# Performance work log

Hardware: AMD Instinct MI355X
Metric: run time of the kernel (lower is better)

## Reference

```python
import jax, jax.numpy as jnp
import numpy as np

# Clause structure: 4 unary clauses and 4 binary (joined-space) clauses,
# each with 3 literals; first literal negated ('n' prefix).
U_IDX = np.array([[0, 1, 2], [3, 4, 5], [6, 7, 8], [9, 10, 11]], dtype=np.int32)
U_SIGNS = np.array([[-1.0, 1.0, 1.0]] * 4, dtype=np.float32)
# Joined matrix columns: [u[i1] (0..15), u[i2] (16..31), binary (32..35)]
B_IDX = np.array([[0, 16, 32], [1, 17, 33], [2, 18, 34], [3, 19, 35]], dtype=np.int32)
B_SIGNS = np.array([[-1.0, 1.0, 1.0]] * 4, dtype=np.float32)

N_NODES, N_UNARY = 50000, 16
N_EDGES, N_BINARY = 1600000, 4
INIT_W = 0.5


def setup_inputs() -> dict:
    key = jax.random.key(0)
    k1, k2, k3, k4 = jax.random.split(key, 4)
    unary = jax.random.normal(k1, (N_NODES, N_UNARY), dtype=jnp.float32)
    binary = jax.random.normal(k2, (N_EDGES, N_BINARY), dtype=jnp.float32)
    edge_index = jax.random.randint(k3, (2, N_EDGES), 0, N_NODES, dtype=jnp.int32)
    wu = jnp.full((4,), INIT_W, dtype=jnp.float32)  # learnable unary clause weights
    wb = jnp.full((4,), INIT_W, dtype=jnp.float32)  # learnable binary clause weights
    return {"unary": unary, "binary": binary, "wu": wu, "wb": wb, "edge_index": edge_index}


def _knowledge_enhancer(x, idx, signs, w):
    """x: [R, P]; idx/signs: [C, L]; w: [C]. Returns summed deltas [R, P]."""
    lit = x[:, idx] * signs                                    # [R, C, L] signed literals
    d = (w[:, None] * jax.nn.softmax(lit, axis=-1)) * signs    # [R, C, L] signed deltas
    return jnp.zeros_like(x).at[:, idx].add(d)                 # scatter-sum over clauses


def reference(unary, binary, wu, wb, edge_index):
    i1, i2 = edge_index[0], edge_index[1]
    P = unary.shape[1]
    # Unary knowledge enhancement
    u = unary + _knowledge_enhancer(unary, U_IDX, U_SIGNS, wu)
    # Join: per-edge [u[i1] | u[i2] | binary]
    joined = jnp.concatenate([u[i1], u[i2], binary], axis=1)   # [E, 2P+B]
    d = _knowledge_enhancer(joined, B_IDX, B_SIGNS, wb)        # [E, 2P+B]
    # GroupBy: scatter node blocks back, keep binary block
    n = unary.shape[0]
    delta_up = (jax.ops.segment_sum(d[:, :P], i1, num_segments=n)
                + jax.ops.segment_sum(d[:, P:2 * P], i2, num_segments=n))
    delta_bp = d[:, 2 * P:]
    # activation = identity (default)
    return u + delta_up, binary + delta_bp
```

## Files before the change

kernel.cpp:

```cpp
#include <hip/hip_runtime.h>
#include <hip/hip_bf16.h>

#define N_NODES 50000
#define N_UNARY 16
#define N_EDGES 1600000
#define N_BINARY 4

typedef float vfloat4 __attribute__((ext_vector_type(4)));

#define FP_SCALE 127.0f
#define FP_INV   (1.0f / 127.0f)

#define BUCKET_SHIFT 11
#define BUCKET_NODES 2048
#define N_BUCKETS 25
#define N_GROUPS 50
#define SEG_CAP 73728
#define N_CHUNKS 10

#define SCAT_BLOCK 1024
#define SCAT_RECS (2 * SCAT_BLOCK)

#define SEG_BYTES  ((size_t)N_GROUPS * SEG_CAP * 8)
#define PART_BYTES ((size_t)N_GROUPS * N_CHUNKS * BUCKET_NODES * 8)
#define WS_NEEDED  (SEG_BYTES + 256 + PART_BYTES)

__device__ inline void enhance_u4(const float x[6], float wu0, float wu1,
                                  float u[4]) {
    float l0 = -x[0], l1 = x[1], l2 = x[2];
    float m  = fmaxf(l0, fmaxf(l1, l2));
    float e0 = __expf(l0 - m), e1 = __expf(l1 - m), e2 = __expf(l2 - m);
    float inv = 1.0f / (e0 + e1 + e2);
    u[0] = x[0] - wu0 * e0 * inv;
    u[1] = x[1] + wu0 * e1 * inv;
    u[2] = x[2] + wu0 * e2 * inv;
    float l3 = -x[3], l4 = x[4], l5 = x[5];
    float m2 = fmaxf(l3, fmaxf(l4, l5));
    float f0 = __expf(l3 - m2), f1 = __expf(l4 - m2), f2 = __expf(l5 - m2);
    float inv2 = 1.0f / (f0 + f1 + f2);
    u[3] = x[3] - wu1 * f0 * inv2;
}

__device__ inline void edge_math(const float* unary, const float* binary,
                                 float wu0, float wu1, const float wc[4],
                                 int i1, int i2, int e,
                                 float s0[4], float s1[4],
                                 float* out_b) {
    const float4* u1p = (const float4*)(unary + (size_t)i1 * N_UNARY);
    const float4* u2p = (const float4*)(unary + (size_t)i2 * N_UNARY);
    float4 x1a = u1p[0], x1b = u1p[1];
    float4 x2a = u2p[0], x2b = u2p[1];
    float xa[6] = {x1a.x, x1a.y, x1a.z, x1a.w, x1b.x, x1b.y};
    float xb[6] = {x2a.x, x2a.y, x2a.z, x2a.w, x2b.x, x2b.y};
    float a[4], b[4];
    enhance_u4(xa, wu0, wu1, a);
    enhance_u4(xb, wu0, wu1, b);

    vfloat4 bn = __builtin_nontemporal_load((const vfloat4*)binary + e);
    float bb[4] = {bn.x, bn.y, bn.z, bn.w};
    float ob[4];
#pragma unroll
    for (int c = 0; c < 4; ++c) {
        float l0 = -a[c], l1 = b[c], l2 = bb[c];
        float m  = fmaxf(l0, fmaxf(l1, l2));
        float e0 = __expf(l0 - m);
        float e1 = __expf(l1 - m);
        float e2 = __expf(l2 - m);
        float inv = 1.0f / (e0 + e1 + e2);
        s0[c] = e0 * inv;
        s1[c] = e1 * inv;
        ob[c] = bb[c] + wc[c] * e2 * inv;
    }
    vfloat4 obv = {ob[0], ob[1], ob[2], ob[3]};
    __builtin_nontemporal_store(obv, (vfloat4*)out_b + e);
}

__device__ inline unsigned long long make_rec(const float s[4], int local_id) {
    unsigned v0 = __float2uint_rn(s[0] * FP_SCALE);
    unsigned v1 = __float2uint_rn(s[1] * FP_SCALE);
    unsigned v2 = __float2uint_rn(s[2] * FP_SCALE);
    unsigned v3 = __float2uint_rn(s[3] * FP_SCALE);
    unsigned pl = v0 | (v1 << 7) | (v2 << 14) | (v3 << 21);
    return (unsigned long long)pl | ((unsigned long long)(unsigned)local_id << 28);
}

__device__ inline unsigned long long pack4_16(const float s[4]) {
    unsigned long long a = __float2uint_rn(s[0] * FP_SCALE);
    unsigned long long b = __float2uint_rn(s[1] * FP_SCALE);
    unsigned long long c = __float2uint_rn(s[2] * FP_SCALE);
    unsigned long long d = __float2uint_rn(s[3] * FP_SCALE);
    return a | (b << 16) | (c << 32) | (d << 48);
}

__global__ void __launch_bounds__(SCAT_BLOCK)
kenn_edge_scatter_kernel(const float* __restrict__ unary,
                         const float* __restrict__ binary,
                         const float* __restrict__ wu,
                         const float* __restrict__ wb,
                         const int* __restrict__ edge_index,
                         unsigned long long* __restrict__ segs,
                         unsigned* __restrict__ tails,
                         float* __restrict__ out_b) {
    __shared__ unsigned l_cnt[N_GROUPS];
    __shared__ unsigned l_pref[N_GROUPS + 1];
    __shared__ unsigned l_gbase[N_GROUPS];
    __shared__ unsigned long long staged[SCAT_RECS];
    __shared__ unsigned char staged_g[SCAT_RECS];

    int tid = threadIdx.x;
    if (tid < N_GROUPS) l_cnt[tid] = 0;
    __syncthreads();

    int e = blockIdx.x * SCAT_BLOCK + tid;
    bool valid = (e < N_EDGES);

    int g1 = 0, g2 = 0;
    unsigned pos1 = 0, pos2 = 0;
    unsigned long long rec1 = 0, rec2 = 0;

    if (valid) {
        int i1 = __builtin_nontemporal_load(edge_index + e);
        int i2 = __builtin_nontemporal_load(edge_index + N_EDGES + e);
        float wu0 = wu[0], wu1 = wu[1];
        float wc[4] = {wb[0], wb[1], wb[2], wb[3]};
        float s0[4], s1[4];
        edge_math(unary, binary, wu0, wu1, wc, i1, i2, e, s0, s1, out_b);
        rec1 = make_rec(s0, i1 & (BUCKET_NODES - 1));
        rec2 = make_rec(s1, i2 & (BUCKET_NODES - 1));
        g1 = i1 >> BUCKET_SHIFT;
        g2 = N_BUCKETS + (i2 >> BUCKET_SHIFT);
        pos1 = atomicAdd(&l_cnt[g1], 1u);
        pos2 = atomicAdd(&l_cnt[g2], 1u);
    }
    __syncthreads();

    if (tid == 0) {
        unsigned run = 0;
#pragma unroll
        for (int g = 0; g < N_GROUPS; ++g) { l_pref[g] = run; run += l_cnt[g]; }
        l_pref[N_GROUPS] = run;
    } else if (tid >= 64 && tid < 64 + N_GROUPS) {
        int g = tid - 64;
        unsigned c = l_cnt[g];
        l_gbase[g] = c ? atomicAdd(tails + g, c) : 0u;
    }
    __syncthreads();

    if (valid) {
        unsigned s1p = l_pref[g1] + pos1;
        unsigned s2p = l_pref[g2] + pos2;
        staged[s1p] = rec1;  staged_g[s1p] = (unsigned char)g1;
        staged[s2p] = rec2;  staged_g[s2p] = (unsigned char)g2;
    }
    __syncthreads();

    unsigned total = l_pref[N_GROUPS];
    for (unsigned i = tid; i < total; i += SCAT_BLOCK) {
        unsigned g = staged_g[i];
        unsigned long long rec = staged[i];
        unsigned p = l_gbase[g] + (i - l_pref[g]);
        if (p < SEG_CAP)
            __builtin_nontemporal_store(rec, segs + (size_t)g * SEG_CAP + p);
    }
}

__global__ void __launch_bounds__(512)
kenn_reduce_kernel(const unsigned long long* __restrict__ segs,
                   const unsigned* __restrict__ tails,
                   unsigned long long* __restrict__ partials) {
    __shared__ unsigned long long lacc[BUCKET_NODES];
    int chunk = blockIdx.x;
    int g     = blockIdx.y;
    int tid   = threadIdx.x;

    for (int i = tid; i < BUCKET_NODES; i += blockDim.x) lacc[i] = 0ull;
    __syncthreads();

    unsigned cnt = tails[g];
    if (cnt > SEG_CAP) cnt = SEG_CAP;
    unsigned csz   = (cnt + N_CHUNKS - 1) / N_CHUNKS;
    unsigned start = chunk * csz;
    unsigned end   = start + csz;
    if (end > cnt) end = cnt;

    const unsigned long long* seg = segs + (size_t)g * SEG_CAP;
    for (unsigned i = start + tid; i < end; i += blockDim.x) {
        unsigned long long r = seg[i];
        unsigned id = (unsigned)(r >> 28) & (BUCKET_NODES - 1);
        unsigned pl = (unsigned)r & 0x0FFFFFFFu;
        unsigned long long exp =
            (unsigned long long)(pl & 127u) |
            ((unsigned long long)(pl & (127u << 7))  << 9)  |
            ((unsigned long long)(pl & (127u << 14)) << 18) |
            ((unsigned long long)(pl & (127u << 21)) << 27);
        atomicAdd(&lacc[id], exp);
    }
    __syncthreads();

    unsigned long long* dst =
        partials + ((size_t)g * N_CHUNKS + chunk) * BUCKET_NODES;
    for (int i = tid; i < BUCKET_NODES; i += blockDim.x)
        __builtin_nontemporal_store(lacc[i], dst + i);
}

__global__ void kenn_node_final_kernel(const float* __restrict__ unary,
                                       const float* __restrict__ wu,
                                       const float* __restrict__ wb,
                                       const unsigned long long* __restrict__ partials,
                                       const unsigned long long* __restrict__ accN,
                                       const unsigned long long* __restrict__ accP,
                                       int use_partials,
                                       float* __restrict__ out_u) {
    int node = blockIdx.x * blockDim.x + threadIdx.x;
    if (node >= N_NODES) return;

    const float4* up = (const float4*)(unary + (size_t)node * N_UNARY);
    float4 x0 = up[0], x1 = up[1], x2 = up[2], x3 = up[3];
    float x[16] = {x0.x, x0.y, x0.z, x0.w,
                   x1.x, x1.y, x1.z, x1.w,
                   x2.x, x2.y, x2.z, x2.w,
                   x3.x, x3.y, x3.z, x3.w};
    float wuc[4] = {wu[0], wu[1], wu[2], wu[3]};

    float y[16];
#pragma unroll
    for (int i = 0; i < 16; ++i) y[i] = x[i];

#pragma unroll
    for (int c = 0; c < 4; ++c) {
        float l0 = -x[3 * c + 0];
        float l1 =  x[3 * c + 1];
        float l2 =  x[3 * c + 2];
        float m  = fmaxf(l0, fmaxf(l1, l2));
        float e0 = __expf(l0 - m);
        float e1 = __expf(l1 - m);
        float e2 = __expf(l2 - m);
        float inv = 1.0f / (e0 + e1 + e2);
        y[3 * c + 0] -= wuc[c] * e0 * inv;
        y[3 * c + 1] += wuc[c] * e1 * inv;
        y[3 * c + 2] += wuc[c] * e2 * inv;
    }

    unsigned long long pn, pp;
    if (use_partials) {
        int bucket = node >> BUCKET_SHIFT;
        int local  = node & (BUCKET_NODES - 1);
        const unsigned long long* pN =
            partials + ((size_t)bucket * N_CHUNKS) * BUCKET_NODES + local;
        const unsigned long long* pP =
            partials + ((size_t)(N_BUCKETS + bucket) * N_CHUNKS) * BUCKET_NODES + local;
        pn = 0ull; pp = 0ull;
#pragma unroll
        for (int c = 0; c < N_CHUNKS; ++c) {
            pn += pN[(size_t)c * BUCKET_NODES];
            pp += pP[(size_t)c * BUCKET_NODES];
        }
    } else {
        pn = accN[node];
        pp = accP[node];
    }

    float wbc[4] = {wb[0], wb[1], wb[2], wb[3]};
    y[0] += wbc[0] * ((float)(int)((pp      ) & 0xffff) - (float)(int)((pn      ) & 0xffff)) * FP_INV;
    y[1] += wbc[1] * ((float)(int)((pp >> 16) & 0xffff) - (float)(int)((pn >> 16) & 0xffff)) * FP_INV;
    y[2] += wbc[2] * ((float)(int)((pp >> 32) & 0xffff) - (float)(int)((pn >> 32) & 0xffff)) * FP_INV;
    y[3] += wbc[3] * ((float)(int)((pp >> 48) & 0xffff) - (float)(int)((pn >> 48) & 0xffff)) * FP_INV;

    float4* op = (float4*)(out_u + (size_t)node * N_UNARY);
    op[0] = make_float4(y[0],  y[1],  y[2],  y[3]);
    op[1] = make_float4(y[4],  y[5],  y[6],  y[7]);
    op[2] = make_float4(y[8],  y[9],  y[10], y[11]);
    op[3] = make_float4(y[12], y[13], y[14], y[15]);
}

__global__ void kenn_edge_atomic_kernel(const float* __restrict__ unary,
                                        const float* __restrict__ binary,
                                        const float* __restrict__ wu,
                                        const float* __restrict__ wb,
                                        const int* __restrict__ edge_index,
                                        unsigned long long* __restrict__ accN,
                                        unsigned long long* __restrict__ accP,
                                        float* __restrict__ out_b) {
    int e = blockIdx.x * blockDim.x + threadIdx.x;
    if (e >= N_EDGES) return;
    int i1 = __builtin_nontemporal_load(edge_index + e);
    int i2 = __builtin_nontemporal_load(edge_index + N_EDGES + e);
    float wu0 = wu[0], wu1 = wu[1];
    float wc[4] = {wb[0], wb[1], wb[2], wb[3]};
    float s0[4], s1[4];
    edge_math(unary, binary, wu0, wu1, wc, i1, i2, e, s0, s1, out_b);
    atomicAdd(accN + i1, pack4_16(s0));
    atomicAdd(accP + i2, pack4_16(s1));
}

extern "C" void kernel_launch(void* const* d_in, const int* in_sizes, int n_in,
                              void* d_out, int out_size, void* d_ws, size_t ws_size,
                              hipStream_t stream) {
    const float* unary      = (const float*)d_in[0];
    const float* binary     = (const float*)d_in[1];
    const float* wu         = (const float*)d_in[2];
    const float* wb         = (const float*)d_in[3];
    const int*   edge_index = (const int*)d_in[4];

    float* out_u = (float*)d_out;
    float* out_b = (float*)d_out + (size_t)N_NODES * N_UNARY;

    if (ws_size >= WS_NEEDED) {
        unsigned long long* segs = (unsigned long long*)d_ws;
        unsigned* tails = (unsigned*)((char*)d_ws + SEG_BYTES);
        unsigned long long* partials =
            (unsigned long long*)((char*)d_ws + SEG_BYTES + 256);

        (void)hipMemsetAsync(tails, 0, N_GROUPS * sizeof(unsigned), stream);
        {
            dim3 grid((N_EDGES + SCAT_BLOCK - 1) / SCAT_BLOCK);
            kenn_edge_scatter_kernel<<<grid, dim3(SCAT_BLOCK), 0, stream>>>(
                unary, binary, wu, wb, edge_index, segs, tails, out_b);
        }
        {
            dim3 grid(N_CHUNKS, N_GROUPS);
            kenn_reduce_kernel<<<grid, dim3(512), 0, stream>>>(
                segs, tails, partials);
        }
        {
            dim3 block(256);
            dim3 grid((N_NODES + 255) / 256);
            kenn_node_final_kernel<<<grid, block, 0, stream>>>(
                unary, wu, wb, partials, nullptr, nullptr, 1, out_u);
        }
    } else {
        unsigned long long* accN = (unsigned long long*)d_ws;
        unsigned long long* accP = accN + N_NODES;
        (void)hipMemsetAsync(accN, 0,
                             (size_t)N_NODES * 2 * sizeof(unsigned long long),
                             stream);
        {
            dim3 block(256);
            dim3 grid((N_EDGES + 255) / 256);
            kenn_edge_atomic_kernel<<<grid, block, 0, stream>>>(
                unary, binary, wu, wb, edge_index, accN, accP, out_b);
        }
        {
            dim3 block(256);
            dim3 grid((N_NODES + 255) / 256);
            kenn_node_final_kernel<<<grid, block, 0, stream>>>(
                unary, wu, wb, nullptr, accN, accP, 0, out_u);
        }
    }
}
```

Baseline: 150.3 us.

## Precompute enhanced unary node values once and simplify edge scatter kernel

Adds a pre-kernel that computes the four enhanced unary values per node once and stores them as a float4 array. The edge kernel then gathers one 16-byte vector per endpoint instead of redoing the unary softmax for every edge. The same pre-kernel also zeroes the tail counters, which replaces the separate memset. Other changes: the scatter block shrinks to 512 threads, bounds checks are dropped because the edge count divides evenly, the serial prefix sum becomes a wavefront shuffle scan, and the tail counters are padded to separate cache lines. The cost is one extra kernel launch and an extra node-sized buffer in the workspace.

```diff
diff --git a/kernel.cpp b/kernel.cpp
--- a/kernel.cpp
+++ b/kernel.cpp
@@ -18,12 +18,16 @@
 #define SEG_CAP 73728
 #define N_CHUNKS 10
 
-#define SCAT_BLOCK 1024
+#define TAILS_STRIDE 16
+
+#define SCAT_BLOCK 512
 #define SCAT_RECS (2 * SCAT_BLOCK)
 
-#define SEG_BYTES  ((size_t)N_GROUPS * SEG_CAP * 8)
-#define PART_BYTES ((size_t)N_GROUPS * N_CHUNKS * BUCKET_NODES * 8)
-#define WS_NEEDED  (SEG_BYTES + 256 + PART_BYTES)
+#define SEG_BYTES   ((size_t)N_GROUPS * SEG_CAP * 8)
+#define TAILS_BYTES ((size_t)4096)
+#define PART_BYTES  ((size_t)N_GROUPS * N_CHUNKS * BUCKET_NODES * 8)
+#define UE_BYTES    ((size_t)N_NODES * 16)
+#define WS_NEEDED   (SEG_BYTES + TAILS_BYTES + PART_BYTES + UE_BYTES)
 
 __device__ inline void enhance_u4(const float x[6], float wu0, float wu1,
                                   float u[4]) {
@@ -92,17 +96,32 @@
     return a | (b << 16) | (c << 32) | (d << 48);
 }
 
+__global__ void __launch_bounds__(256)
+kenn_pre_kernel(const float* __restrict__ unary,
+                const float* __restrict__ wu,
+                float4* __restrict__ ue,
+                unsigned* __restrict__ tails) {
+    int n = blockIdx.x * blockDim.x + threadIdx.x;
+    if (n < N_GROUPS) tails[n * TAILS_STRIDE] = 0u;
+    if (n >= N_NODES) return;
+    const float4* up = (const float4*)(unary + (size_t)n * N_UNARY);
+    float4 x0 = up[0], x1 = up[1];
+    float x[6] = {x0.x, x0.y, x0.z, x0.w, x1.x, x1.y};
+    float u[4];
+    enhance_u4(x, wu[0], wu[1], u);
+    ue[n] = make_float4(u[0], u[1], u[2], u[3]);
+}
+
 __global__ void __launch_bounds__(SCAT_BLOCK)
-kenn_edge_scatter_kernel(const float* __restrict__ unary,
+kenn_edge_scatter_kernel(const float4* __restrict__ ue,
                          const float* __restrict__ binary,
-                         const float* __restrict__ wu,
                          const float* __restrict__ wb,
                          const int* __restrict__ edge_index,
                          unsigned long long* __restrict__ segs,
                          unsigned* __restrict__ tails,
                          float* __restrict__ out_b) {
     __shared__ unsigned l_cnt[N_GROUPS];
-    __shared__ unsigned l_pref[N_GROUPS + 1];
+    __shared__ unsigned l_pref[N_GROUPS];
     __shared__ unsigned l_gbase[N_GROUPS];
     __shared__ unsigned long long staged[SCAT_RECS];
     __shared__ unsigned char staged_g[SCAT_RECS];
@@ -112,50 +131,66 @@
     __syncthreads();
 
     int e = blockIdx.x * SCAT_BLOCK + tid;
-    bool valid = (e < N_EDGES);
-
-    int g1 = 0, g2 = 0;
-    unsigned pos1 = 0, pos2 = 0;
-    unsigned long long rec1 = 0, rec2 = 0;
-
-    if (valid) {
-        int i1 = __builtin_nontemporal_load(edge_index + e);
-        int i2 = __builtin_nontemporal_load(edge_index + N_EDGES + e);
-        float wu0 = wu[0], wu1 = wu[1];
-        float wc[4] = {wb[0], wb[1], wb[2], wb[3]};
-        float s0[4], s1[4];
-        edge_math(unary, binary, wu0, wu1, wc, i1, i2, e, s0, s1, out_b);
-        rec1 = make_rec(s0, i1 & (BUCKET_NODES - 1));
-        rec2 = make_rec(s1, i2 & (BUCKET_NODES - 1));
-        g1 = i1 >> BUCKET_SHIFT;
-        g2 = N_BUCKETS + (i2 >> BUCKET_SHIFT);
-        pos1 = atomicAdd(&l_cnt[g1], 1u);
-        pos2 = atomicAdd(&l_cnt[g2], 1u);
-    }
-    __syncthreads();
-
-    if (tid == 0) {
-        unsigned run = 0;
-#pragma unroll
-        for (int g = 0; g < N_GROUPS; ++g) { l_pref[g] = run; run += l_cnt[g]; }
-        l_pref[N_GROUPS] = run;
+    int i1 = __builtin_nontemporal_load(edge_index + e);
+    int i2 = __builtin_nontemporal_load(edge_index + N_EDGES + e);
+
+    float4 av = ue[i1];
+    float4 bv = ue[i2];
+    float a[4] = {av.x, av.y, av.z, av.w};
+    float b[4] = {bv.x, bv.y, bv.z, bv.w};
+    vfloat4 bn = __builtin_nontemporal_load((const vfloat4*)binary + e);
+    float bb[4] = {bn.x, bn.y, bn.z, bn.w};
+    float wc[4] = {wb[0], wb[1], wb[2], wb[3]};
+
+    float s0[4], s1[4], ob[4];
+#pragma unroll
+    for (int c = 0; c < 4; ++c) {
+        float l0 = -a[c], l1 = b[c], l2 = bb[c];
+        float m  = fmaxf(l0, fmaxf(l1, l2));
+        float e0 = __expf(l0 - m);
+        float e1 = __expf(l1 - m);
+        float e2 = __expf(l2 - m);
+        float inv = 1.0f / (e0 + e1 + e2);
+        s0[c] = e0 * inv;
+        s1[c] = e1 * inv;
+        ob[c] = bb[c] + wc[c] * e2 * inv;
+    }
+    vfloat4 obv = {ob[0], ob[1], ob[2], ob[3]};
+    __builtin_nontemporal_store(obv, (vfloat4*)out_b + e);
+
+    unsigned long long rec1 = make_rec(s0, i1 & (BUCKET_NODES - 1));
+    unsigned long long rec2 = make_rec(s1, i2 & (BUCKET_NODES - 1));
+    int g1 = i1 >> BUCKET_SHIFT;
+    int g2 = N_BUCKETS + (i2 >> BUCKET_SHIFT);
+    unsigned pos1 = atomicAdd(&l_cnt[g1], 1u);
+    unsigned pos2 = atomicAdd(&l_cnt[g2], 1u);
+    __syncthreads();
+
+    if (tid < 64) {
+        unsigned c = (tid < N_GROUPS) ? l_cnt[tid] : 0u;
+        unsigned s = c;
+#pragma unroll
+        for (int off = 1; off < 64; off <<= 1) {
+            unsigned o = __shfl_up(s, off, 64);
+            if (tid >= off) s += o;
+        }
+        if (tid < N_GROUPS) l_pref[tid] = s - c;
     } else if (tid >= 64 && tid < 64 + N_GROUPS) {
         int g = tid - 64;
         unsigned c = l_cnt[g];
-        l_gbase[g] = c ? atomicAdd(tails + g, c) : 0u;
-    }
-    __syncthreads();
-
-    if (valid) {
-        unsigned s1p = l_pref[g1] + pos1;
-        unsigned s2p = l_pref[g2] + pos2;
-        staged[s1p] = rec1;  staged_g[s1p] = (unsigned char)g1;
-        staged[s2p] = rec2;  staged_g[s2p] = (unsigned char)g2;
-    }
-    __syncthreads();
-
-    unsigned total = l_pref[N_GROUPS];
-    for (unsigned i = tid; i < total; i += SCAT_BLOCK) {
+        l_gbase[g] = c ? atomicAdd(tails + g * TAILS_STRIDE, c) : 0u;
+    }
+    __syncthreads();
+
+    unsigned p1 = l_pref[g1] + pos1;
+    unsigned p2 = l_pref[g2] + pos2;
+    staged[p1] = rec1;  staged_g[p1] = (unsigned char)g1;
+    staged[p2] = rec2;  staged_g[p2] = (unsigned char)g2;
+    __syncthreads();
+
+#pragma unroll
+    for (int k = 0; k < 2; ++k) {
+        unsigned i = (unsigned)tid + k * SCAT_BLOCK;
         unsigned g = staged_g[i];
         unsigned long long rec = staged[i];
         unsigned p = l_gbase[g] + (i - l_pref[g]);
@@ -176,7 +211,7 @@
     for (int i = tid; i < BUCKET_NODES; i += blockDim.x) lacc[i] = 0ull;
     __syncthreads();
 
-    unsigned cnt = tails[g];
+    unsigned cnt = tails[g * TAILS_STRIDE];
     if (cnt > SEG_CAP) cnt = SEG_CAP;
     unsigned csz   = (cnt + N_CHUNKS - 1) / N_CHUNKS;
     unsigned start = chunk * csz;
@@ -309,13 +344,18 @@
         unsigned long long* segs = (unsigned long long*)d_ws;
         unsigned* tails = (unsigned*)((char*)d_ws + SEG_BYTES);
         unsigned long long* partials =
-            (unsigned long long*)((char*)d_ws + SEG_BYTES + 256);
-
-        (void)hipMemsetAsync(tails, 0, N_GROUPS * sizeof(unsigned), stream);
-        {
-            dim3 grid((N_EDGES + SCAT_BLOCK - 1) / SCAT_BLOCK);
+            (unsigned long long*)((char*)d_ws + SEG_BYTES + TAILS_BYTES);
+        float4* ue =
+            (float4*)((char*)d_ws + SEG_BYTES + TAILS_BYTES + PART_BYTES);
+
+        {
+            dim3 grid((N_NODES + 255) / 256);
+            kenn_pre_kernel<<<grid, dim3(256), 0, stream>>>(unary, wu, ue, tails);
+        }
+        {
+            dim3 grid(N_EDGES / SCAT_BLOCK);
             kenn_edge_scatter_kernel<<<grid, dim3(SCAT_BLOCK), 0, stream>>>(
-                unary, binary, wu, wb, edge_index, segs, tails, out_b);
+                ue, binary, wb, edge_index, segs, tails, out_b);
         }
         {
             dim3 grid(N_CHUNKS, N_GROUPS);
```

New measurement: 172.6 us. +14.8%, slower.
